# Optimization experiments

Measured on AMD Instinct MI355X. Metric: run time of the kernel, lower is better.

Reference implementation:

```python
import jax, jax.numpy as jnp
import numpy as np

K = 3
STRIDE = 1
PADDING = 1
INVALID = -1.0


def _unfold(x, k, stride, padding, fill):
    # x: [B, C, H, W] -> patches [B, C, k, k, P] matching torch F.unfold ordering
    x = jnp.pad(x, ((0, 0), (0, 0), (padding, padding), (padding, padding)),
                constant_values=fill)
    # feature dim ordered channel-major (C, kh, kw), same as torch unfold
    p = jax.lax.conv_general_dilated_patches(x, (k, k), (stride, stride), 'VALID')
    b, _, ho, wo = p.shape
    c = x.shape[1]
    return p.reshape(b, c, k, k, ho * wo), ho, wo


def setup_inputs() -> dict:
    key = jax.random.key(0)
    k1, k2, k3, k4 = jax.random.split(key, 4)
    B, C, H, W = 8, 64, 128, 128
    OC = 64
    inp = jax.random.normal(k1, (B, C, H, W), dtype=jnp.float32)
    mask = jax.random.randint(k2, (B, H, W), 0, 4).astype(jnp.float32)
    conv = jax.random.normal(k3, (OC, C, K, K), dtype=jnp.float32) * 0.05
    bias = jax.random.normal(k4, (OC,), dtype=jnp.float32) * 0.05
    return {"inp": inp, "mask": mask, "conv": conv, "bias": bias}


def reference(inp, mask, conv, bias):
    k, stride, padding = K, STRIDE, PADDING
    b, c, h_in, w_in = inp.shape
    oc = conv.shape[0]
    center = (k - 1) // 2

    inp_patched, ho, wo = _unfold(inp, k, stride, padding, INVALID)       # [B,C,k,k,P]
    mask_patched, _, _ = _unfold(mask[:, None], k, stride, padding, INVALID)  # [B,1,k,k,P]
    mask_patched = mask_patched[:, 0]                                      # [B,k,k,P]

    center_val = mask_patched[:, center:center + 1, center:center + 1, :]  # [B,1,1,P]
    mask_eq = (mask_patched == center_val).astype(inp.dtype)               # [B,k,k,P]

    masked_input = inp_patched * mask_eq[:, None]                          # [B,C,k,k,P]
    m_norm = (k * k) / jnp.clip(mask_eq.reshape(b, k * k, -1).sum(axis=1), 1e-8)  # [B,P]

    masked_input = masked_input.reshape(b, c, k * k, -1)                   # [B,C,kk,P]
    w = conv.reshape(oc, c, k * k)                                         # [O,C,kk]
    out = jnp.einsum('bcxp,ocx->bop', masked_input, w)                     # [B,O,P]
    out = out * m_norm[:, None, :]
    out = out.reshape(b, oc, ho, wo)
    out = out + bias[None, :, None, None]

    mask_out = mask_patched[:, center, center, :].reshape(b, 1, ho, wo)
    return out, mask_out
```

## Files before the change

### kernel.cpp

```cpp
#include <hip/hip_runtime.h>
#include <stdint.h>

#define HW   128
#define CIN  64
#define OCN  64
#define NB   8

typedef __attribute__((ext_vector_type(8)))  short short8;
typedef __attribute__((ext_vector_type(16))) float floatx16;
typedef unsigned long long u64;

union F8 { short8 s; u64 u[2]; uint32_t d[4]; };

static __device__ __forceinline__ ushort f2bf(float f) {
    uint32_t u = __float_as_uint(f);
    uint32_t r = (u + 0x7FFFu + ((u >> 16) & 1u)) >> 16;
    return (ushort)r;
}

__global__ void wprep_kernel(const float* __restrict__ conv, ushort* __restrict__ wb) {
    int idx = blockIdx.x * 256 + threadIdx.x;
    int tap = idx >> 12;
    int r   = idx & 4095;
    int oc  = r >> 6;
    int c   = r & 63;
    wb[idx] = f2bf(conv[(oc * 64 + c) * 9 + tap]);
}

#define XS_CSTR 68
#define XS_ROW  (HW * XS_CSTR)
#define AS_STR  68
#define LDS_BYTES 80640

__global__ __launch_bounds__(256, 2)
void iconv_main(const float* __restrict__ inp, const float* __restrict__ mask,
                const ushort* __restrict__ wb, const float* __restrict__ bias,
                float* __restrict__ out)
{
    extern __shared__ char smem[];
    ushort* Xs = (ushort*)smem;
    ushort* As = Xs + 4 * XS_ROW;
    float*  Ms = (float*)(smem + 78336);
    float*  Bb = (float*)(smem + 78336 + 2048);

    const int tid  = threadIdx.x;
    const int bb   = blockIdx.x >> 6;
    const int y0   = (blockIdx.x & 63) << 1;
    const int lane = tid & 63;
    const int l31  = lane & 31;
    const int lh   = lane >> 5;
    const int w    = tid >> 6;
    const int yloc = w >> 1;
    const int xw   = (w & 1) * 64;
    const int y    = y0 + yloc;

    {
        const int cp = tid & 31;
        const int xq = (tid >> 5) * 16;
        const float* base0 = inp + ((size_t)(bb * CIN + 2 * cp) * HW) * HW;
        #pragma unroll
        for (int rr = 0; rr < 4; ++rr) {
            int gy = y0 - 1 + rr;
            if (gy >= 0 && gy < HW) {
                const float4* q0 = (const float4*)(base0 + (size_t)gy * HW + xq);
                const float4* q1 = (const float4*)(base0 + (size_t)HW * HW + (size_t)gy * HW + xq);
                float4 v0[4], v1[4];
                #pragma unroll
                for (int i = 0; i < 4; ++i) { v0[i] = q0[i]; v1[i] = q1[i]; }
                ushort* xrow = Xs + rr * XS_ROW + xq * XS_CSTR + 2 * cp;
                const float* f0 = (const float*)v0;
                const float* f1 = (const float*)v1;
                #pragma unroll
                for (int i = 0; i < 16; ++i) {
                    uint32_t p = (uint32_t)f2bf(f0[i]) | ((uint32_t)f2bf(f1[i]) << 16);
                    *(uint32_t*)(xrow + i * XS_CSTR) = p;
                }
            }
        }
    }
    {
        int rr = tid >> 6, x0 = (tid & 63) * 2;
        int gy = y0 - 1 + rr;
        if (gy >= 0 && gy < HW) {
            float2 v = *(const float2*)(mask + ((size_t)bb * HW + gy) * HW + x0);
            Ms[rr * HW + x0]     = v.x;
            Ms[rr * HW + x0 + 1] = v.y;
        }
    }
    if (tid < OCN) Bb[tid] = bias[tid];

    uint4 wv0 = *(const uint4*)(wb + tid * 16);
    uint4 wv1 = *(const uint4*)(wb + tid * 16 + 8);

    __syncthreads();

    uint32_t sel[9][2];
    float norm0, norm1;
    {
        int cnt0 = 0, cnt1 = 0;
        int xq0 = xw + l31, xq1 = xw + 32 + l31;
        float m00 = Ms[(1 + yloc) * HW + xq0];
        float m01 = Ms[(1 + yloc) * HW + xq1];
        #pragma unroll
        for (int t = 0; t < 9; ++t) {
            int dy = t / 3 - 1, dx = t % 3 - 1;
            int ny = y + dy;
            bool vy = (ny >= 0) && (ny < HW);
            int rbase = (1 + yloc + dy) * HW;
            {
                int nx = xq0 + dx;
                bool ok = vy && (nx >= 0) && (nx < HW);
                int nxc = nx < 0 ? 0 : (nx > HW - 1 ? HW - 1 : nx);
                bool eq = ok && (Ms[rbase + nxc] == m00);
                sel[t][0] = eq ? 0xFFFFFFFFu : 0u;
                cnt0 += eq ? 1 : 0;
            }
            {
                int nx = xq1 + dx;
                bool ok = vy && (nx >= 0) && (nx < HW);
                int nxc = nx < 0 ? 0 : (nx > HW - 1 ? HW - 1 : nx);
                bool eq = ok && (Ms[rbase + nxc] == m01);
                sel[t][1] = eq ? 0xFFFFFFFFu : 0u;
                cnt1 += eq ? 1 : 0;
            }
        }
        norm0 = 9.0f / (float)cnt0;
        norm1 = 9.0f / (float)cnt1;
    }

    floatx16 acc00 = {0,0,0,0,0,0,0,0,0,0,0,0,0,0,0,0};
    floatx16 acc01 = {0,0,0,0,0,0,0,0,0,0,0,0,0,0,0,0};
    floatx16 acc10 = {0,0,0,0,0,0,0,0,0,0,0,0,0,0,0,0};
    floatx16 acc11 = {0,0,0,0,0,0,0,0,0,0,0,0,0,0,0,0};

    const ushort* A0p = As + l31 * AS_STR + lh * 8;
    const ushort* A1p = As + (l31 + 32) * AS_STR + lh * 8;

    #pragma unroll
    for (int t = 0; t < 9; ++t) {
        if (t > 0) __syncthreads();
        {
            int oc = tid >> 2, c0 = (tid & 3) << 4;
            ushort* dst = As + oc * AS_STR + c0;
            *(uint2*)(dst)      = make_uint2(wv0.x, wv0.y);
            *(uint2*)(dst + 4)  = make_uint2(wv0.z, wv0.w);
            *(uint2*)(dst + 8)  = make_uint2(wv1.x, wv1.y);
            *(uint2*)(dst + 12) = make_uint2(wv1.z, wv1.w);
        }
        if (t < 8) {
            wv0 = *(const uint4*)(wb + (t + 1) * 4096 + tid * 16);
            wv1 = *(const uint4*)(wb + (t + 1) * 4096 + tid * 16 + 8);
        }
        __syncthreads();

        const int dy = t / 3 - 1, dx = t % 3 - 1;
        const int rrB = 1 + yloc + dy;
        int xa = xw + l31 + dx;
        int xb0c = xa < 0 ? 0 : (xa > HW - 1 ? HW - 1 : xa);
        int xa1 = xa + 32;
        int xb1c = xa1 < 0 ? 0 : (xa1 > HW - 1 ? HW - 1 : xa1);
        const ushort* B0p = Xs + rrB * XS_ROW + xb0c * XS_CSTR + lh * 8;
        const ushort* B1p = Xs + rrB * XS_ROW + xb1c * XS_CSTR + lh * 8;
        const uint32_t s0 = sel[t][0], s1 = sel[t][1];

        #pragma unroll
        for (int ks = 0; ks < 4; ++ks) {
            F8 a0, a1, b0, b1;
            a0.u[0] = *(const u64*)(A0p + ks * 16);
            a0.u[1] = *(const u64*)(A0p + ks * 16 + 4);
            a1.u[0] = *(const u64*)(A1p + ks * 16);
            a1.u[1] = *(const u64*)(A1p + ks * 16 + 4);
            b0.u[0] = *(const u64*)(B0p + ks * 16);
            b0.u[1] = *(const u64*)(B0p + ks * 16 + 4);
            b1.u[0] = *(const u64*)(B1p + ks * 16);
            b1.u[1] = *(const u64*)(B1p + ks * 16 + 4);
            b0.d[0] &= s0; b0.d[1] &= s0; b0.d[2] &= s0; b0.d[3] &= s0;
            b1.d[0] &= s1; b1.d[1] &= s1; b1.d[2] &= s1; b1.d[3] &= s1;
            acc00 = __builtin_amdgcn_mfma_f32_32x32x16_bf16(a0.s, b0.s, acc00, 0, 0, 0);
            acc01 = __builtin_amdgcn_mfma_f32_32x32x16_bf16(a0.s, b1.s, acc01, 0, 0, 0);
            acc10 = __builtin_amdgcn_mfma_f32_32x32x16_bf16(a1.s, b0.s, acc10, 0, 0, 0);
            acc11 = __builtin_amdgcn_mfma_f32_32x32x16_bf16(a1.s, b1.s, acc11, 0, 0, 0);
        }
    }

    float* outp = out + (size_t)bb * OCN * HW * HW + (size_t)y * HW;
    #pragma unroll
    for (int mt = 0; mt < 2; ++mt) {
        #pragma unroll
        for (int nt = 0; nt < 2; ++nt) {
            floatx16 a = (mt == 0) ? (nt == 0 ? acc00 : acc01)
                                   : (nt == 0 ? acc10 : acc11);
            float nm = (nt == 0) ? norm0 : norm1;
            int x = xw + nt * 32 + l31;
            #pragma unroll
            for (int r = 0; r < 16; ++r) {
                int oc = mt * 32 + (r & 3) + 8 * (r >> 2) + 4 * lh;
                outp[(size_t)oc * (HW * HW) + x] = a[r] * nm + Bb[oc];
            }
        }
    }
}

extern "C" void kernel_launch(void* const* d_in, const int* in_sizes, int n_in,
                              void* d_out, int out_size, void* d_ws, size_t ws_size,
                              hipStream_t stream) {
    (void)in_sizes; (void)n_in; (void)out_size; (void)ws_size;
    const float* inp  = (const float*)d_in[0];
    const float* mask = (const float*)d_in[1];
    const float* conv = (const float*)d_in[2];
    const float* bias = (const float*)d_in[3];
    float* out = (float*)d_out;
    ushort* wb = (ushort*)d_ws;

    hipFuncSetAttribute((const void*)iconv_main,
                        hipFuncAttributeMaxDynamicSharedMemorySize, LDS_BYTES);

    wprep_kernel<<<144, 256, 0, stream>>>(conv, wb);
    iconv_main<<<NB * (HW / 2), 256, LDS_BYTES, stream>>>(inp, mask, wb, bias, out);

    hipMemcpyAsync(out + (size_t)NB * OCN * HW * HW, mask,
                   (size_t)NB * HW * HW * sizeof(float),
                   hipMemcpyDeviceToDevice, stream);
}
```

Before: 104.9 us.

## Load weights directly into registers and fuse mask copy into main kernel

Weight fragments now go from global memory straight into a double-buffered register array, prefetched one tap ahead, instead of being staged through LDS. This removes the two per-tap __syncthreads and the LDS weight buffer, which also shrinks the LDS footprint. The separate device-to-device memcpy of the mask output is folded into the main kernel, with each block writing its two rows. The cost is 64 extra VGPRs for the weight buffers, which could cause spills under launch_bounds(256,2), and weight reads that repeat per wave from L2.

```diff
diff --git a/kernel.cpp b/kernel.cpp
--- a/kernel.cpp
+++ b/kernel.cpp
@@ -10,7 +10,7 @@
 typedef __attribute__((ext_vector_type(16))) float floatx16;
 typedef unsigned long long u64;
 
-union F8 { short8 s; u64 u[2]; uint32_t d[4]; };
+union F8 { short8 s; u64 u[2]; uint32_t d[4]; uint4 q; };
 
 static __device__ __forceinline__ ushort f2bf(float f) {
     uint32_t u = __float_as_uint(f);
@@ -29,8 +29,7 @@
 
 #define XS_CSTR 68
 #define XS_ROW  (HW * XS_CSTR)
-#define AS_STR  68
-#define LDS_BYTES 80640
+#define LDS_BYTES 72192
 
 __global__ __launch_bounds__(256, 2)
 void iconv_main(const float* __restrict__ inp, const float* __restrict__ mask,
@@ -39,9 +38,8 @@
 {
     extern __shared__ char smem[];
     ushort* Xs = (ushort*)smem;
-    ushort* As = Xs + 4 * XS_ROW;
-    float*  Ms = (float*)(smem + 78336);
-    float*  Bb = (float*)(smem + 78336 + 2048);
+    float*  Ms = (float*)(smem + 69632);
+    float*  Bb = (float*)(smem + 69632 + 2048);
 
     const int tid  = threadIdx.x;
     const int bb   = blockIdx.x >> 6;
@@ -89,8 +87,19 @@
     }
     if (tid < OCN) Bb[tid] = bias[tid];
 
-    uint4 wv0 = *(const uint4*)(wb + tid * 16);
-    uint4 wv1 = *(const uint4*)(wb + tid * 16 + 8);
+    {
+        int r = tid >> 7, x = tid & 127;
+        int gy = y0 + r;
+        out[(size_t)NB * OCN * HW * HW + ((size_t)bb * HW + gy) * HW + x] =
+            mask[((size_t)bb * HW + gy) * HW + x];
+    }
+
+    uint4 Areg[2][8];
+    #pragma unroll
+    for (int i = 0; i < 8; ++i) {
+        int h = i >> 2, ks = i & 3;
+        Areg[0][i] = *(const uint4*)(wb + (l31 + h * 32) * 64 + ks * 16 + lh * 8);
+    }
 
     __syncthreads();
 
@@ -133,25 +142,17 @@
     floatx16 acc10 = {0,0,0,0,0,0,0,0,0,0,0,0,0,0,0,0};
     floatx16 acc11 = {0,0,0,0,0,0,0,0,0,0,0,0,0,0,0,0};
 
-    const ushort* A0p = As + l31 * AS_STR + lh * 8;
-    const ushort* A1p = As + (l31 + 32) * AS_STR + lh * 8;
-
     #pragma unroll
     for (int t = 0; t < 9; ++t) {
-        if (t > 0) __syncthreads();
-        {
-            int oc = tid >> 2, c0 = (tid & 3) << 4;
-            ushort* dst = As + oc * AS_STR + c0;
-            *(uint2*)(dst)      = make_uint2(wv0.x, wv0.y);
-            *(uint2*)(dst + 4)  = make_uint2(wv0.z, wv0.w);
-            *(uint2*)(dst + 8)  = make_uint2(wv1.x, wv1.y);
-            *(uint2*)(dst + 12) = make_uint2(wv1.z, wv1.w);
-        }
+        const int buf = t & 1, nbuf = buf ^ 1;
         if (t < 8) {
-            wv0 = *(const uint4*)(wb + (t + 1) * 4096 + tid * 16);
-            wv1 = *(const uint4*)(wb + (t + 1) * 4096 + tid * 16 + 8);
-        }
-        __syncthreads();
+            const ushort* wp = wb + (t + 1) * 4096;
+            #pragma unroll
+            for (int i = 0; i < 8; ++i) {
+                int h = i >> 2, ks = i & 3;
+                Areg[nbuf][i] = *(const uint4*)(wp + (l31 + h * 32) * 64 + ks * 16 + lh * 8);
+            }
+        }
 
         const int dy = t / 3 - 1, dx = t % 3 - 1;
         const int rrB = 1 + yloc + dy;
@@ -166,10 +167,8 @@
         #pragma unroll
         for (int ks = 0; ks < 4; ++ks) {
             F8 a0, a1, b0, b1;
-            a0.u[0] = *(const u64*)(A0p + ks * 16);
-            a0.u[1] = *(const u64*)(A0p + ks * 16 + 4);
-            a1.u[0] = *(const u64*)(A1p + ks * 16);
-            a1.u[1] = *(const u64*)(A1p + ks * 16 + 4);
+            a0.q = Areg[buf][ks];
+            a1.q = Areg[buf][4 + ks];
             b0.u[0] = *(const u64*)(B0p + ks * 16);
             b0.u[1] = *(const u64*)(B0p + ks * 16 + 4);
             b1.u[0] = *(const u64*)(B1p + ks * 16);
@@ -217,8 +216,4 @@
 
     wprep_kernel<<<144, 256, 0, stream>>>(conv, wb);
     iconv_main<<<NB * (HW / 2), 256, LDS_BYTES, stream>>>(inp, mask, wb, bias, out);
-
-    hipMemcpyAsync(out + (size_t)NB * OCN * HW * HW, mask,
-                   (size_t)NB * HW * HW * sizeof(float),
-                   hipMemcpyDeviceToDevice, stream);
-}
+}
```

Result: slower. 110.5 us (+5.4%).
